# Kernel tuning notes

Hardware: AMD Instinct MI355X
Metric: run time of the kernel (lower is better)

Reference implementation:

```python
import jax, jax.numpy as jnp
import numpy as np

QUERY = 1024
VALUE = 1024
HID = 1024
SEQ = 2048
BATCH = 64
INIT_RANGE = 0.1


def setup_inputs() -> dict:
    key = jax.random.key(0)
    ks = jax.random.split(key, 5)
    q = jax.random.normal(ks[0], (BATCH, QUERY), dtype=jnp.float32)
    v = jax.random.normal(ks[1], (SEQ, BATCH, VALUE), dtype=jnp.float32)
    u = lambda k, shape: jax.random.uniform(k, shape, jnp.float32, -INIT_RANGE, INIT_RANGE)
    W_v = u(ks[2], (HID, VALUE))
    b_v = jnp.zeros((HID,), jnp.float32)
    W_q = u(ks[3], (HID, QUERY))
    b_q = jnp.zeros((HID,), jnp.float32)
    W_o = u(ks[4], (1, HID))
    b_o = jnp.zeros((1,), jnp.float32)
    return {"q": q, "v": v, "W_v": W_v, "b_v": b_v, "W_q": W_q, "b_q": b_q, "W_o": W_o, "b_o": b_o}


def reference(q, v, W_v, b_v, W_q, b_q, W_o, b_o):
    # v: [S, B, V] -> [B, S, V]
    vt = jnp.transpose(v, (1, 0, 2))
    h_v = jnp.einsum('bsv,hv->bsh', vt, W_v) + b_v          # [B, S, H]
    h_q = jnp.einsum('bq,hq->bh', q, W_q) + b_q              # [B, H]
    h = jnp.tanh(h_v + h_q[:, None, :])                      # [B, S, H]
    logit = jnp.einsum('bsh,h->bs', h, W_o[0]) + b_o[0]      # [B, S]
    logit = logit - jnp.max(logit, axis=1, keepdims=True)
    p = jax.nn.softmax(logit, axis=1)                        # [B, S]
    ctx = jnp.sum(vt * p[:, :, None], axis=1, keepdims=True) # [B, 1, V]
    out = jnp.transpose(ctx, (1, 0, 2))                      # [1, B, V]
    return (out, p)
```

## Files before the change

kernel.cpp:

```cpp
#include <hip/hip_runtime.h>
#include <hip/hip_bf16.h>
#include <stdint.h>

#define BATCH 64
#define SEQ   2048
#define VDIM  1024
#define HDIM  1024

typedef __bf16 b8v __attribute__((ext_vector_type(8)));
typedef __bf16 b4v __attribute__((ext_vector_type(4)));
typedef float f32x4 __attribute__((ext_vector_type(4)));
typedef unsigned short u16x8 __attribute__((ext_vector_type(8)));

__device__ __forceinline__ float bf2f(unsigned short u) {
    union { unsigned int i; float f; } cv; cv.i = ((unsigned int)u) << 16; return cv.f;
}

__device__ __forceinline__ unsigned int pack_bf16_2(float a, float b) {
#if __has_builtin(__builtin_amdgcn_cvt_pk_bf16_f32)
    auto t = __builtin_amdgcn_cvt_pk_bf16_f32(a, b);
    unsigned int r; __builtin_memcpy(&r, &t, 4); return r;
#else
    union { float f; unsigned int u; } ca, cb; ca.f = a; cb.f = b;
    unsigned int ra = ca.u + 0x7FFF + ((ca.u >> 16) & 1);
    unsigned int rb = cb.u + 0x7FFF + ((cb.u >> 16) & 1);
    return (ra >> 16) | (rb & 0xFFFF0000u);
#endif
}

__device__ __forceinline__ void gload_lds16(const unsigned short* g, unsigned short* l) {
    __builtin_amdgcn_global_load_lds(
        (const __attribute__((address_space(1))) unsigned int*)g,
        (__attribute__((address_space(3))) unsigned int*)l, 16, 0, 0);
}

__global__ __launch_bounds__(256) void cvt_bf16_kernel(
    const float* __restrict__ in, unsigned short* __restrict__ out, long n4)
{
    long g = (long)blockIdx.x * 256 + threadIdx.x;
    if (g >= n4) return;
    float4 a = *(const float4*)(in + g * 4);
    b4v o = {(__bf16)a.x, (__bf16)a.y, (__bf16)a.z, (__bf16)a.w};
    *(b4v*)(out + g * 4) = o;
}

__global__ __launch_bounds__(256) void hq_kernel(
    const float* __restrict__ q, const float* __restrict__ Wq,
    const float* __restrict__ bq, const float* __restrict__ bv,
    float* __restrict__ hq)
{
    int g = blockIdx.x * 256 + threadIdx.x;
    int b = g >> 10, h = g & 1023;
    const float4* qr = (const float4*)(q + ((size_t)b << 10));
    const float4* wr = (const float4*)(Wq + ((size_t)h << 10));
    float acc = 0.f;
    #pragma unroll 8
    for (int k = 0; k < 256; ++k) {
        float4 qa = qr[k], wa = wr[k];
        acc += qa.x*wa.x + qa.y*wa.y + qa.z*wa.z + qa.w*wa.w;
    }
    hq[g] = acc + bq[h] + bv[h];
}

#define GEMM_EPILOGUE()                                                        \
    float rowsum[4][4];                                                        \
    _Pragma("unroll") for (int i = 0; i < 4; ++i)                              \
        _Pragma("unroll") for (int r = 0; r < 4; ++r) rowsum[i][r] = 0.f;      \
    _Pragma("unroll") for (int j = 0; j < 4; ++j) {                            \
        const int h = n_tile*128 + wave_n + j*16 + col;                        \
        const float wo = Wo[h];                                                \
        _Pragma("unroll") for (int i = 0; i < 4; ++i) {                        \
            const int brow = i*16 + quad*4;                                    \
            _Pragma("unroll") for (int r = 0; r < 4; ++r) {                    \
                float x = acc[i][j][r] + hq[(brow + r)*HDIM + h];              \
                float t = __expf(2.f * x);                                     \
                rowsum[i][r] += wo * (1.f - 2.f / (t + 1.f));                  \
            }                                                                  \
        }                                                                      \
    }                                                                          \
    _Pragma("unroll") for (int off = 1; off < 16; off <<= 1)                   \
        _Pragma("unroll") for (int i = 0; i < 4; ++i)                          \
            _Pragma("unroll") for (int r = 0; r < 4; ++r)                      \
                rowsum[i][r] += __shfl_xor(rowsum[i][r], off, 64);             \
    if (col == 0) {                                                            \
        _Pragma("unroll") for (int i = 0; i < 4; ++i)                          \
            _Pragma("unroll") for (int r = 0; r < 4; ++r)                      \
                atomicAdd(&logit_lds[wave_m + i*16 + quad*4 + r], rowsum[i][r]); \
    }                                                                          \
    __syncthreads();                                                           \
    if (tid < 128) {                                                           \
        const int b = tid & 63;                                                \
        const int s = m_tile*2 + (tid >> 6);                                   \
        atomicAdd(&logit[b*SEQ + s], logit_lds[tid]);                          \
    }

__global__ __launch_bounds__(256) void fused_bf16(
    const unsigned short* __restrict__ v, const unsigned short* __restrict__ Wv,
    const float* __restrict__ Wo, const float* __restrict__ hq,
    float* __restrict__ logit)
{
    __shared__ __align__(16) unsigned short ldsA[128*32];
    __shared__ __align__(16) unsigned short ldsB[128*32];
    __shared__ float logit_lds[128];

    const int tid  = threadIdx.x;
    const int w    = tid >> 6;
    const int lane = tid & 63;
    const int col  = lane & 15;
    const int quad = lane >> 4;
    const int wave_m = (w >> 1) << 6;
    const int wave_n = (w & 1) << 6;
    const int n_tile = blockIdx.x;
    const int m_tile = blockIdx.y;

    if (tid < 128) logit_lds[tid] = 0.f;

    f32x4 acc[4][4];
    #pragma unroll
    for (int i = 0; i < 4; ++i)
        #pragma unroll
        for (int j = 0; j < 4; ++j) acc[i][j] = (f32x4)(0.f);

    const int srow = (w << 5) + (lane >> 2);
    const int scol = (lane & 3) << 3;
    const unsigned short* gA = v  + (size_t)(m_tile * 128 + srow) * VDIM + scol;
    const unsigned short* gB = Wv + (size_t)(n_tile * 128 + srow) * VDIM + scol;
    unsigned short* lA = ldsA + (w << 10) + (lane << 3);
    unsigned short* lB = ldsB + (w << 10) + (lane << 3);

    for (int kt = 0; kt < 32; ++kt) {
        const int ko = kt << 5;
        __syncthreads();
        gload_lds16(gA + ko,           lA);
        gload_lds16(gA + ko + 16*VDIM, lA + 512);
        gload_lds16(gB + ko,           lB);
        gload_lds16(gB + ko + 16*VDIM, lB + 512);
        __syncthreads();

        b8v aF[4], bF[4];
        #pragma unroll
        for (int i = 0; i < 4; ++i)
            aF[i] = *(const b8v*)(ldsA + ((wave_m + i*16 + col) << 5) + (quad << 3));
        #pragma unroll
        for (int j = 0; j < 4; ++j)
            bF[j] = *(const b8v*)(ldsB + ((wave_n + j*16 + col) << 5) + (quad << 3));
        #pragma unroll
        for (int i = 0; i < 4; ++i)
            #pragma unroll
            for (int j = 0; j < 4; ++j)
                acc[i][j] = __builtin_amdgcn_mfma_f32_16x16x32_bf16(aF[i], bF[j], acc[i][j], 0, 0, 0);
    }

    GEMM_EPILOGUE()
}

__global__ __launch_bounds__(256) void fused_f32(
    const float* __restrict__ v, const float* __restrict__ Wv,
    const float* __restrict__ Wo, const float* __restrict__ hq,
    float* __restrict__ logit)
{
    __shared__ __align__(16) unsigned short ldsA[128*32];
    __shared__ __align__(16) unsigned short ldsB[128*32];
    __shared__ float logit_lds[128];

    const int tid  = threadIdx.x;
    const int w    = tid >> 6;
    const int lane = tid & 63;
    const int col  = lane & 15;
    const int quad = lane >> 4;
    const int wave_m = (w >> 1) << 6;
    const int wave_n = (w & 1) << 6;
    const int n_tile = blockIdx.x;
    const int m_tile = blockIdx.y;

    if (tid < 128) logit_lds[tid] = 0.f;

    f32x4 acc[4][4];
    #pragma unroll
    for (int i = 0; i < 4; ++i)
        #pragma unroll
        for (int j = 0; j < 4; ++j) acc[i][j] = (f32x4)(0.f);

    const int srow8 = lane >> 3;
    const int scolf = (lane & 7) << 2;
    const float* gA = v  + (size_t)(m_tile * 128 + w*32 + srow8) * VDIM + scolf;
    const float* gB = Wv + (size_t)(n_tile * 128 + w*32 + srow8) * VDIM + scolf;
    unsigned short* lA = ldsA + (w*32 + srow8)*32 + ((lane & 7) << 2);
    unsigned short* lB = ldsB + (w*32 + srow8)*32 + ((lane & 7) << 2);

    float4 ra[4], rb[4];
    #pragma unroll
    for (int r = 0; r < 4; ++r) {
        ra[r] = *(const float4*)(gA + r*8*VDIM);
        rb[r] = *(const float4*)(gB + r*8*VDIM);
    }

    for (int kt = 0; kt < 32; ++kt) {
        __syncthreads();
        #pragma unroll
        for (int r = 0; r < 4; ++r) {
            uint2 pa = { pack_bf16_2(ra[r].x, ra[r].y), pack_bf16_2(ra[r].z, ra[r].w) };
            uint2 pb = { pack_bf16_2(rb[r].x, rb[r].y), pack_bf16_2(rb[r].z, rb[r].w) };
            *(uint2*)(lA + r*256) = pa;
            *(uint2*)(lB + r*256) = pb;
        }
        __syncthreads();

        if (kt < 31) {
            const int ko = (kt + 1) << 5;
            #pragma unroll
            for (int r = 0; r < 4; ++r) {
                ra[r] = *(const float4*)(gA + ko + r*8*VDIM);
                rb[r] = *(const float4*)(gB + ko + r*8*VDIM);
            }
        }

        b8v aF[4], bF[4];
        #pragma unroll
        for (int i = 0; i < 4; ++i)
            aF[i] = *(const b8v*)(ldsA + ((wave_m + i*16 + col) << 5) + (quad << 3));
        #pragma unroll
        for (int j = 0; j < 4; ++j)
            bF[j] = *(const b8v*)(ldsB + ((wave_n + j*16 + col) << 5) + (quad << 3));
        #pragma unroll
        for (int i = 0; i < 4; ++i)
            #pragma unroll
            for (int j = 0; j < 4; ++j)
                acc[i][j] = __builtin_amdgcn_mfma_f32_16x16x32_bf16(aF[i], bF[j], acc[i][j], 0, 0, 0);
    }

    GEMM_EPILOGUE()
}

__global__ __launch_bounds__(256) void softmax_kernel(float* __restrict__ logit,
                                                      float* __restrict__ pout)
{
    const int b = blockIdx.x, tid = threadIdx.x;
    float* row = logit + b * SEQ;
    __shared__ float red[4];

    float e[8];
    float lmax = -1e30f;
    #pragma unroll
    for (int k = 0; k < 8; ++k) { e[k] = row[tid + k*256]; lmax = fmaxf(lmax, e[k]); }
    #pragma unroll
    for (int off = 32; off > 0; off >>= 1) lmax = fmaxf(lmax, __shfl_xor(lmax, off, 64));
    if ((tid & 63) == 0) red[tid >> 6] = lmax;
    __syncthreads();
    lmax = fmaxf(fmaxf(red[0], red[1]), fmaxf(red[2], red[3]));
    __syncthreads();
    float lsum = 0.f;
    #pragma unroll
    for (int k = 0; k < 8; ++k) { e[k] = __expf(e[k] - lmax); lsum += e[k]; }
    #pragma unroll
    for (int off = 32; off > 0; off >>= 1) lsum += __shfl_xor(lsum, off, 64);
    if ((tid & 63) == 0) red[tid >> 6] = lsum;
    __syncthreads();
    lsum = red[0] + red[1] + red[2] + red[3];
    const float inv = 1.f / lsum;
    #pragma unroll
    for (int k = 0; k < 8; ++k) {
        const int s = tid + k*256;
        const float pv = e[k] * inv;
        row[s] = pv;
        pout[b*SEQ + s] = pv;
    }
}

__global__ __launch_bounds__(128) void ctx_f32(
    const float* __restrict__ v, const float* __restrict__ p, float* __restrict__ ctx)
{
    const int b = blockIdx.y, sc = blockIdx.x, tid = threadIdx.x;
    float acc[8];
    #pragma unroll
    for (int e = 0; e < 8; ++e) acc[e] = 0.f;
    for (int s = sc*128; s < sc*128 + 128; ++s) {
        const float pv = p[b*SEQ + s];
        const float4* vp = (const float4*)(v + (size_t)(s*64 + b) * VDIM + tid*8);
        float4 v0 = vp[0], v1 = vp[1];
        acc[0] = fmaf(pv, v0.x, acc[0]); acc[1] = fmaf(pv, v0.y, acc[1]);
        acc[2] = fmaf(pv, v0.z, acc[2]); acc[3] = fmaf(pv, v0.w, acc[3]);
        acc[4] = fmaf(pv, v1.x, acc[4]); acc[5] = fmaf(pv, v1.y, acc[5]);
        acc[6] = fmaf(pv, v1.z, acc[6]); acc[7] = fmaf(pv, v1.w, acc[7]);
    }
    #pragma unroll
    for (int e = 0; e < 8; ++e) atomicAdd(&ctx[b*VDIM + tid*8 + e], acc[e]);
}

__global__ __launch_bounds__(128) void ctx_bf16(
    const unsigned short* __restrict__ v, const float* __restrict__ p, float* __restrict__ ctx)
{
    const int b = blockIdx.y, sc = blockIdx.x, tid = threadIdx.x;
    float acc[8];
    #pragma unroll
    for (int e = 0; e < 8; ++e) acc[e] = 0.f;
    for (int s = sc*128; s < sc*128 + 128; ++s) {
        const float pv = p[b*SEQ + s];
        u16x8 val = *(const u16x8*)(v + (size_t)(s*64 + b) * VDIM + tid*8);
        #pragma unroll
        for (int e = 0; e < 8; ++e) acc[e] = fmaf(pv, bf2f(val[e]), acc[e]);
    }
    #pragma unroll
    for (int e = 0; e < 8; ++e) atomicAdd(&ctx[b*VDIM + tid*8 + e], acc[e]);
}

__global__ __launch_bounds__(256) void copy_kernel(const float* __restrict__ src,
                                                   float* __restrict__ dst)
{
    int g = blockIdx.x * 256 + threadIdx.x;
    dst[g] = src[g];
}

extern "C" void kernel_launch(void* const* d_in, const int* in_sizes, int n_in,
                              void* d_out, int out_size, void* d_ws, size_t ws_size,
                              hipStream_t stream)
{
    const float* q  = (const float*)d_in[0];
    const float* v  = (const float*)d_in[1];
    const float* Wv = (const float*)d_in[2];
    const float* bv = (const float*)d_in[3];
    const float* Wq = (const float*)d_in[4];
    const float* bq = (const float*)d_in[5];
    const float* Wo = (const float*)d_in[6];

    float* hq_ws    = (float*)d_ws;
    float* logit_ws = hq_ws + 65536;
    float* ctx_ws   = logit_ws + 131072;
    unsigned short* vb  = (unsigned short*)(ctx_ws + 65536);
    unsigned short* Wvb = vb + (size_t)SEQ*BATCH*VDIM;

    const size_t needA = (size_t)(65536 + 131072 + 65536) * 4
                       + ((size_t)SEQ*BATCH*VDIM + (size_t)HDIM*VDIM) * 2;
    const bool bigws = ws_size >= needA;

    float* out_ctx = (float*)d_out;
    float* out_p   = out_ctx + 65536;

    hipMemsetAsync(logit_ws, 0, (131072 + 65536) * sizeof(float), stream);
    hq_kernel<<<256, 256, 0, stream>>>(q, Wq, bq, bv, hq_ws);

    if (bigws) {
        cvt_bf16_kernel<<<(SEQ*BATCH*VDIM/4 + 255)/256, 256, 0, stream>>>(v,  vb,  (long)SEQ*BATCH*VDIM/4);
        cvt_bf16_kernel<<<(HDIM*VDIM/4 + 255)/256,      256, 0, stream>>>(Wv, Wvb, (long)HDIM*VDIM/4);
        fused_bf16<<<dim3(8, 1024), 256, 0, stream>>>(vb, Wvb, Wo, hq_ws, logit_ws);
        softmax_kernel<<<64, 256, 0, stream>>>(logit_ws, out_p);
        ctx_bf16<<<dim3(16, 64), 128, 0, stream>>>(vb, logit_ws, ctx_ws);
    } else {
        fused_f32<<<dim3(8, 1024), 256, 0, stream>>>(v, Wv, Wo, hq_ws, logit_ws);
        softmax_kernel<<<64, 256, 0, stream>>>(logit_ws, out_p);
        ctx_f32<<<dim3(16, 64), 128, 0, stream>>>(v, logit_ws, ctx_ws);
    }
    copy_kernel<<<256, 256, 0, stream>>>(ctx_ws, out_ctx);
}
```

Baseline: 1.324 ms.

## Replace bf16 GEMM with triple-buffered 128x256 pipelined kernel and trim auxiliary kernels

Replaces the 128x128 single-buffered bf16 fused GEMM with a 512-thread, 128x256-tile kernel. It uses a triple-buffered LDS ring with XOR-swizzled global-to-LDS loads, split prefetch across two half-phases, and s_setprio around the MFMA blocks. Block IDs are remapped so that concurrently running blocks share Wv tiles. The change also widens the bf16 conversion to 8 elements per thread, coalesces hq_kernel over batch, and has the ctx kernel accumulate directly into the output, dropping the copy kernel. These aim to hide load latency and cut launch and memory overhead, at the cost of more LDS per block and hand-tuned waitcnt logic that must stay exactly right.

```diff
diff --git a/kernel.cpp b/kernel.cpp
--- a/kernel.cpp
+++ b/kernel.cpp
@@ -6,6 +6,7 @@
 #define SEQ   2048
 #define VDIM  1024
 #define HDIM  1024
+#define LDSB  24576
 
 typedef __bf16 b8v __attribute__((ext_vector_type(8)));
 typedef __bf16 b4v __attribute__((ext_vector_type(4)));
@@ -35,13 +36,15 @@
 }
 
 __global__ __launch_bounds__(256) void cvt_bf16_kernel(
-    const float* __restrict__ in, unsigned short* __restrict__ out, long n4)
+    const float* __restrict__ in, unsigned short* __restrict__ out, long n8)
 {
     long g = (long)blockIdx.x * 256 + threadIdx.x;
-    if (g >= n4) return;
-    float4 a = *(const float4*)(in + g * 4);
-    b4v o = {(__bf16)a.x, (__bf16)a.y, (__bf16)a.z, (__bf16)a.w};
-    *(b4v*)(out + g * 4) = o;
+    if (g >= n8) return;
+    float4 a = *(const float4*)(in + g * 8);
+    float4 b = *(const float4*)(in + g * 8 + 4);
+    b8v o = {(__bf16)a.x, (__bf16)a.y, (__bf16)a.z, (__bf16)a.w,
+             (__bf16)b.x, (__bf16)b.y, (__bf16)b.z, (__bf16)b.w};
+    *(b8v*)(out + g * 8) = o;
 }
 
 __global__ __launch_bounds__(256) void hq_kernel(
@@ -49,17 +52,173 @@
     const float* __restrict__ bq, const float* __restrict__ bv,
     float* __restrict__ hq)
 {
-    int g = blockIdx.x * 256 + threadIdx.x;
-    int b = g >> 10, h = g & 1023;
-    const float4* qr = (const float4*)(q + ((size_t)b << 10));
+    const int h = blockIdx.x * 4 + (threadIdx.x >> 6);
+    const int lane = threadIdx.x & 63;
+    const float4* qr = (const float4*)(q + ((size_t)lane << 10));
     const float4* wr = (const float4*)(Wq + ((size_t)h << 10));
     float acc = 0.f;
     #pragma unroll 8
     for (int k = 0; k < 256; ++k) {
-        float4 qa = qr[k], wa = wr[k];
+        float4 wa = wr[k];
+        float4 qa = qr[k];
         acc += qa.x*wa.x + qa.y*wa.y + qa.z*wa.z + qa.w*wa.w;
     }
-    hq[g] = acc + bq[h] + bv[h];
+    hq[((size_t)lane << 10) + h] = acc + bq[h] + bv[h];
+}
+
+__global__ __launch_bounds__(512, 2) void fused_8ph(
+    const unsigned short* __restrict__ v, const unsigned short* __restrict__ Wv,
+    const float* __restrict__ Wo, const float* __restrict__ hq,
+    float* __restrict__ logit)
+{
+    __shared__ __align__(16) unsigned short lds[3 * LDSB];
+    __shared__ float logit_lds[128];
+
+    const int tid  = threadIdx.x;
+    const int w    = tid >> 6;
+    const int lane = tid & 63;
+    const int col  = lane & 15;
+    const int quad = lane >> 4;
+    const int wm   = w >> 2;
+    const int wn   = w & 3;
+
+    const int bid    = blockIdx.x;
+    const int work   = ((bid & 7) << 9) + (bid >> 3);
+    const int m_tile = work >> 2;
+    const int n_tile = work & 3;
+
+    if (tid < 128) logit_lds[tid] = 0.f;
+
+    f32x4 acc[4][4];
+    #pragma unroll
+    for (int i = 0; i < 4; ++i)
+        #pragma unroll
+        for (int j = 0; j < 4; ++j) acc[i][j] = (f32x4)(0.f);
+
+    const int rowoff = tid >> 3;
+    const int ch     = (tid & 7) ^ (rowoff & 7);
+    const unsigned short* gA = v  + (size_t)(m_tile * 128 + rowoff) * VDIM + (ch << 3);
+    const unsigned short* gB = Wv + (size_t)(n_tile * 256 + rowoff) * VDIM + (ch << 3);
+    const int ldA = tid << 3;
+    const int ldB = 8192 + (tid << 3);
+
+    gload_lds16(gA,                  lds + ldA);
+    gload_lds16(gA + 64*VDIM,        lds + 4096 + ldA);
+    gload_lds16(gB,                  lds + ldB);
+    gload_lds16(gB + 64*VDIM,        lds + 4096 + ldB);
+    gload_lds16(gB + 128*VDIM,       lds + 8192 + ldB);
+    gload_lds16(gB + 192*VDIM,       lds + 12288 + ldB);
+    gload_lds16(gA + 64,             lds + LDSB + ldA);
+    gload_lds16(gA + 64 + 64*VDIM,   lds + LDSB + 4096 + ldA);
+    gload_lds16(gB + 64,             lds + LDSB + ldB);
+    gload_lds16(gB + 64 + 64*VDIM,   lds + LDSB + 4096 + ldB);
+    gload_lds16(gB + 64 + 128*VDIM,  lds + LDSB + 8192 + ldB);
+    gload_lds16(gB + 64 + 192*VDIM,  lds + LDSB + 12288 + ldB);
+    asm volatile("s_waitcnt vmcnt(6)" ::: "memory");
+    __builtin_amdgcn_s_barrier();
+
+    const int aoffbase = (wm * 64 + col) * 64;
+    const int boffbase = 8192 + (wn * 64 + col) * 64;
+    const int axor     = col & 7;
+
+    const unsigned short* gAs = gA + 128;
+    const unsigned short* gBs = gB + 128;
+    int cbase = 0;
+    int sbase = 2 * LDSB;
+
+    b8v aF[4], bF[4];
+
+#define FRAG_LOAD(kkc)                                                          \
+    {   const int co = ((((kkc) << 2) + quad) ^ axor) << 3;                     \
+        _Pragma("unroll") for (int i = 0; i < 4; ++i)                           \
+            aF[i] = *(const b8v*)(lds + cbase + aoffbase + i*1024 + co);        \
+        _Pragma("unroll") for (int j = 0; j < 4; ++j)                           \
+            bF[j] = *(const b8v*)(lds + cbase + boffbase + j*1024 + co);    }
+
+#define MFMA16()                                                                \
+    _Pragma("unroll") for (int i = 0; i < 4; ++i)                               \
+        _Pragma("unroll") for (int j = 0; j < 4; ++j)                           \
+            acc[i][j] = __builtin_amdgcn_mfma_f32_16x16x32_bf16(aF[i], bF[j], acc[i][j], 0, 0, 0);
+
+    #pragma unroll 1
+    for (int t = 0; t < 16; ++t) {
+        FRAG_LOAD(0)
+        if (t < 14) {
+            gload_lds16(gAs,            lds + sbase + ldA);
+            gload_lds16(gAs + 64*VDIM,  lds + sbase + 4096 + ldA);
+            gload_lds16(gBs,            lds + sbase + ldB);
+        }
+        __builtin_amdgcn_s_barrier();
+        asm volatile("s_waitcnt lgkmcnt(0)" ::: "memory");
+        __builtin_amdgcn_sched_barrier(0);
+        __builtin_amdgcn_s_setprio(1);
+        MFMA16()
+        __builtin_amdgcn_s_setprio(0);
+        __builtin_amdgcn_s_barrier();
+
+        FRAG_LOAD(1)
+        if (t < 14) {
+            gload_lds16(gBs + 64*VDIM,   lds + sbase + 4096 + ldB);
+            gload_lds16(gBs + 128*VDIM,  lds + sbase + 8192 + ldB);
+            gload_lds16(gBs + 192*VDIM,  lds + sbase + 12288 + ldB);
+        }
+        __builtin_amdgcn_s_barrier();
+        asm volatile("s_waitcnt lgkmcnt(0)" ::: "memory");
+        __builtin_amdgcn_sched_barrier(0);
+        __builtin_amdgcn_s_setprio(1);
+        MFMA16()
+        __builtin_amdgcn_s_setprio(0);
+        if (t <= 13)      { asm volatile("s_waitcnt vmcnt(6)" ::: "memory"); }
+        else if (t == 14) { asm volatile("s_waitcnt vmcnt(0)" ::: "memory"); }
+        __builtin_amdgcn_s_barrier();
+
+        gAs += 64; gBs += 64;
+        cbase += LDSB; if (cbase == 3 * LDSB) cbase = 0;
+        sbase += LDSB; if (sbase == 3 * LDSB) sbase = 0;
+    }
+#undef FRAG_LOAD
+#undef MFMA16
+
+    float rowsum[4][4];
+    #pragma unroll
+    for (int i = 0; i < 4; ++i)
+        #pragma unroll
+        for (int r = 0; r < 4; ++r) rowsum[i][r] = 0.f;
+    #pragma unroll
+    for (int j = 0; j < 4; ++j) {
+        const int h = n_tile * 256 + wn * 64 + j * 16 + col;
+        const float wo = Wo[h];
+        #pragma unroll
+        for (int i = 0; i < 4; ++i) {
+            const int brow = i * 16 + quad * 4;
+            #pragma unroll
+            for (int r = 0; r < 4; ++r) {
+                float x = acc[i][j][r] + hq[(brow + r) * HDIM + h];
+                float t = __expf(2.f * x);
+                rowsum[i][r] += wo * (1.f - 2.f / (t + 1.f));
+            }
+        }
+    }
+    #pragma unroll
+    for (int off = 1; off < 16; off <<= 1)
+        #pragma unroll
+        for (int i = 0; i < 4; ++i)
+            #pragma unroll
+            for (int r = 0; r < 4; ++r)
+                rowsum[i][r] += __shfl_xor(rowsum[i][r], off, 64);
+    if (col == 0) {
+        #pragma unroll
+        for (int i = 0; i < 4; ++i)
+            #pragma unroll
+            for (int r = 0; r < 4; ++r)
+                atomicAdd(&logit_lds[wm * 64 + i * 16 + quad * 4 + r], rowsum[i][r]);
+    }
+    __syncthreads();
+    if (tid < 128) {
+        const int b = tid & 63;
+        const int s = m_tile * 2 + (tid >> 6);
+        atomicAdd(&logit[b * SEQ + s], logit_lds[tid]);
+    }
 }
 
 #define GEMM_EPILOGUE()                                                        \
@@ -94,8 +253,8 @@
         atomicAdd(&logit[b*SEQ + s], logit_lds[tid]);                          \
     }
 
-__global__ __launch_bounds__(256) void fused_bf16(
-    const unsigned short* __restrict__ v, const unsigned short* __restrict__ Wv,
+__global__ __launch_bounds__(256) void fused_f32(
+    const float* __restrict__ v, const float* __restrict__ Wv,
     const float* __restrict__ Wo, const float* __restrict__ hq,
     float* __restrict__ logit)
 {
@@ -121,66 +280,6 @@
         #pragma unroll
         for (int j = 0; j < 4; ++j) acc[i][j] = (f32x4)(0.f);
 
-    const int srow = (w << 5) + (lane >> 2);
-    const int scol = (lane & 3) << 3;
-    const unsigned short* gA = v  + (size_t)(m_tile * 128 + srow) * VDIM + scol;
-    const unsigned short* gB = Wv + (size_t)(n_tile * 128 + srow) * VDIM + scol;
-    unsigned short* lA = ldsA + (w << 10) + (lane << 3);
-    unsigned short* lB = ldsB + (w << 10) + (lane << 3);
-
-    for (int kt = 0; kt < 32; ++kt) {
-        const int ko = kt << 5;
-        __syncthreads();
-        gload_lds16(gA + ko,           lA);
-        gload_lds16(gA + ko + 16*VDIM, lA + 512);
-        gload_lds16(gB + ko,           lB);
-        gload_lds16(gB + ko + 16*VDIM, lB + 512);
-        __syncthreads();
-
-        b8v aF[4], bF[4];
-        #pragma unroll
-        for (int i = 0; i < 4; ++i)
-            aF[i] = *(const b8v*)(ldsA + ((wave_m + i*16 + col) << 5) + (quad << 3));
-        #pragma unroll
-        for (int j = 0; j < 4; ++j)
-            bF[j] = *(const b8v*)(ldsB + ((wave_n + j*16 + col) << 5) + (quad << 3));
-        #pragma unroll
-        for (int i = 0; i < 4; ++i)
-            #pragma unroll
-            for (int j = 0; j < 4; ++j)
-                acc[i][j] = __builtin_amdgcn_mfma_f32_16x16x32_bf16(aF[i], bF[j], acc[i][j], 0, 0, 0);
-    }
-
-    GEMM_EPILOGUE()
-}
-
-__global__ __launch_bounds__(256) void fused_f32(
-    const float* __restrict__ v, const float* __restrict__ Wv,
-    const float* __restrict__ Wo, const float* __restrict__ hq,
-    float* __restrict__ logit)
-{
-    __shared__ __align__(16) unsigned short ldsA[128*32];
-    __shared__ __align__(16) unsigned short ldsB[128*32];
-    __shared__ float logit_lds[128];
-
-    const int tid  = threadIdx.x;
-    const int w    = tid >> 6;
-    const int lane = tid & 63;
-    const int col  = lane & 15;
-    const int quad = lane >> 4;
-    const int wave_m = (w >> 1) << 6;
-    const int wave_n = (w & 1) << 6;
-    const int n_tile = blockIdx.x;
-    const int m_tile = blockIdx.y;
-
-    if (tid < 128) logit_lds[tid] = 0.f;
-
-    f32x4 acc[4][4];
-    #pragma unroll
-    for (int i = 0; i < 4; ++i)
-        #pragma unroll
-        for (int j = 0; j < 4; ++j) acc[i][j] = (f32x4)(0.f);
-
     const int srow8 = lane >> 3;
     const int scolf = (lane & 7) << 2;
     const float* gA = v  + (size_t)(m_tile * 128 + w*32 + srow8) * VDIM + scolf;
@@ -304,13 +403,6 @@
     for (int e = 0; e < 8; ++e) atomicAdd(&ctx[b*VDIM + tid*8 + e], acc[e]);
 }
 
-__global__ __launch_bounds__(256) void copy_kernel(const float* __restrict__ src,
-                                                   float* __restrict__ dst)
-{
-    int g = blockIdx.x * 256 + threadIdx.x;
-    dst[g] = src[g];
-}
-
 extern "C" void kernel_launch(void* const* d_in, const int* in_sizes, int n_in,
                               void* d_out, int out_size, void* d_ws, size_t ws_size,
                               hipStream_t stream)
@@ -336,19 +428,19 @@
     float* out_ctx = (float*)d_out;
     float* out_p   = out_ctx + 65536;
 
-    hipMemsetAsync(logit_ws, 0, (131072 + 65536) * sizeof(float), stream);
+    hipMemsetAsync(logit_ws, 0, 131072 * sizeof(float), stream);
+    hipMemsetAsync(out_ctx, 0, 65536 * sizeof(float), stream);
     hq_kernel<<<256, 256, 0, stream>>>(q, Wq, bq, bv, hq_ws);
 
     if (bigws) {
-        cvt_bf16_kernel<<<(SEQ*BATCH*VDIM/4 + 255)/256, 256, 0, stream>>>(v,  vb,  (long)SEQ*BATCH*VDIM/4);
-        cvt_bf16_kernel<<<(HDIM*VDIM/4 + 255)/256,      256, 0, stream>>>(Wv, Wvb, (long)HDIM*VDIM/4);
-        fused_bf16<<<dim3(8, 1024), 256, 0, stream>>>(vb, Wvb, Wo, hq_ws, logit_ws);
+        cvt_bf16_kernel<<<65536, 256, 0, stream>>>(v,  vb,  (long)SEQ*BATCH*VDIM/8);
+        cvt_bf16_kernel<<<512,   256, 0, stream>>>(Wv, Wvb, (long)HDIM*VDIM/8);
+        fused_8ph<<<4096, 512, 0, stream>>>(vb, Wvb, Wo, hq_ws, logit_ws);
         softmax_kernel<<<64, 256, 0, stream>>>(logit_ws, out_p);
-        ctx_bf16<<<dim3(16, 64), 128, 0, stream>>>(vb, logit_ws, ctx_ws);
+        ctx_bf16<<<dim3(16, 64), 128, 0, stream>>>(vb, logit_ws, out_ctx);
     } else {
         fused_f32<<<dim3(8, 1024), 256, 0, stream>>>(v, Wv, Wo, hq_ws, logit_ws);
         softmax_kernel<<<64, 256, 0, stream>>>(logit_ws, out_p);
-        ctx_f32<<<dim3(16, 64), 128, 0, stream>>>(v, logit_ws, ctx_ws);
-    }
-    copy_kernel<<<256, 256, 0, stream>>>(ctx_ws, out_ctx);
-}
+        ctx_f32<<<dim3(16, 64), 128, 0, stream>>>(v, logit_ws, out_ctx);
+    }
+}
```

Measured after the change: 1.258 ms. 5.0% less time.
